# Optimization experiments

Hardware: AMD Instinct MI355X
Metric: run time of the kernel (lower is better)

## Reference

```python
import jax, jax.numpy as jnp
import numpy as np


def setup_inputs() -> dict:
    key = jax.random.key(0)
    k1, k2 = jax.random.split(key)
    B, N, T, D = 16, 2048, 168, 64
    spatial_nodes = jax.random.normal(k1, (B, N, D), dtype=jnp.float32)
    temporal_nodes = jax.random.normal(k2, (B, T, D), dtype=jnp.float32)
    return {"spatial_nodes": spatial_nodes, "temporal_nodes": temporal_nodes}


def reference(spatial_nodes, temporal_nodes):
    # node_embs: [B, N+T, D]
    node_embs = jnp.concatenate([spatial_nodes, temporal_nodes], axis=1)
    # Dense pairwise similarity, then tanh(relu(.)) threshold.
    # batch_adj: [B, N+T, N+T]
    batch_adj = jnp.einsum('bnf,bmf->bnm', node_embs, node_embs)
    batch_adj = jnp.tanh(jax.nn.relu(batch_adj))
    # The torch module additionally extracts per-batch variable-length
    # edge lists (nonzero indices + weights) from batch_adj; those are a
    # pure re-indexing of batch_adj with data-dependent shapes, so the
    # jit-compatible reference returns the dense adjacency, from which
    # edge lists are trivially recoverable (nonzero entries of batch_adj).
    return batch_adj
```

## Files before the change

kernel.cpp:

```cpp
#include <hip/hip_runtime.h>
#include <stdint.h>


constexpr int Bsz = 16;
constexpr int Nsp = 2048;
constexpr int Ttm = 168;
constexpr int D   = 64;
constexpr int M   = Nsp + Ttm;
constexpr int NG32 = (M + 31) / 32;
constexpr int NG   = 72;
constexpr int GRP_SH   = 4 * 64 * 8;
constexpr int BATCH_SH = NG * GRP_SH;
constexpr int PLANE_SH = Bsz * BATCH_SH;
constexpr size_t WS_NEED = (size_t)2 * PLANE_SH * sizeof(unsigned short);

typedef __attribute__((ext_vector_type(8)))  short bf16x8;
typedef __attribute__((ext_vector_type(16))) float f32x16;

__device__ inline void split8(const float4& a, const float4& b,
                              bf16x8& hi, bf16x8& lo) {
    float x[8] = {a.x, a.y, a.z, a.w, b.x, b.y, b.z, b.w};
    #pragma unroll
    for (int i = 0; i < 8; ++i) {
        union { float f; uint32_t u; } v; v.f = x[i];
        uint32_t hu = (v.u + 0x7FFFu + ((v.u >> 16) & 1u)) >> 16;
        union { uint32_t u; float f; } hf; hf.u = hu << 16;
        union { float f; uint32_t u; } r; r.f = x[i] - hf.f;
        uint32_t lu = (r.u + 0x7FFFu + ((r.u >> 16) & 1u)) >> 16;
        hi[i] = (short)hu;
        lo[i] = (short)lu;
    }
}

__device__ inline float act_tanh_relu(float x) {
    const float xr = fmaxf(x, 0.0f);
    const float e  = __expf(2.0f * xr);
    const float r  = __builtin_amdgcn_rcpf(e + 1.0f);
    return 1.0f - 2.0f * r;
}

__global__ __launch_bounds__(256) void convert_kernel(
    const float* __restrict__ spatial,
    const float* __restrict__ temporal,
    unsigned short* __restrict__ ws)
{
    const int idx = blockIdx.x * 256 + threadIdx.x;
    const int b  = idx / (NG * 4 * 64);
    const int r1 = idx % (NG * 4 * 64);
    const int g  = r1 / (4 * 64);
    const int r2 = r1 % (4 * 64);
    const int ks   = r2 >> 6;
    const int lane = r2 & 63;
    const int row  = 32 * g + (lane & 31);
    const int k0   = ks * 16 + 8 * (lane >> 5);

    float4 v0 = make_float4(0.f, 0.f, 0.f, 0.f), v1 = v0;
    if (row < M) {
        const float* src = (row < Nsp)
            ? spatial  + ((size_t)b * Nsp + row) * D
            : temporal + ((size_t)b * Ttm + (row - Nsp)) * D;
        v0 = *(const float4*)(src + k0);
        v1 = *(const float4*)(src + k0 + 4);
    }
    bf16x8 hi, lo;
    split8(v0, v1, hi, lo);

    const size_t o = (size_t)b * BATCH_SH + (size_t)g * GRP_SH + (ks * 64 + lane) * 8;
    *(bf16x8*)(ws + o)            = hi;
    *(bf16x8*)(ws + PLANE_SH + o) = lo;
}

__global__ __launch_bounds__(256, 4) void stgraph_rowpanel(
    const unsigned short* __restrict__ ws,
    float* __restrict__ out)
{
    const int tid = threadIdx.x;
    const int g   = blockIdx.x;
    const int b   = blockIdx.y;

    const int lane = tid & 63;
    const int w    = tid >> 6;
    const int l31  = lane & 31;
    const int lhi  = lane >> 5;

    const unsigned short* Hb = ws + (size_t)b * BATCH_SH;
    const unsigned short* Lb = Hb + PLANE_SH;

    bf16x8 ahi[4], alo[4];
    #pragma unroll
    for (int ks = 0; ks < 4; ++ks) {
        const int fo = (ks * 64 + lane) * 8;
        ahi[ks] = *(const bf16x8*)(Hb + (size_t)g * GRP_SH + fo);
        alo[ks] = *(const bf16x8*)(Lb + (size_t)g * GRP_SH + fo);
    }

    float* out_b = out + (size_t)b * M * M;

    for (int ct = w; ct < NG32; ct += 4) {
        f32x16 acc = {};
        #pragma unroll
        for (int ks = 0; ks < 4; ++ks) {
            const int fo = (ks * 64 + lane) * 8;
            bf16x8 bhi = *(const bf16x8*)(Hb + (size_t)ct * GRP_SH + fo);
            bf16x8 blo = *(const bf16x8*)(Lb + (size_t)ct * GRP_SH + fo);
            acc = __builtin_amdgcn_mfma_f32_32x32x16_bf16(ahi[ks], bhi, acc, 0, 0, 0);
            acc = __builtin_amdgcn_mfma_f32_32x32x16_bf16(ahi[ks], blo, acc, 0, 0, 0);
            acc = __builtin_amdgcn_mfma_f32_32x32x16_bf16(alo[ks], bhi, acc, 0, 0, 0);
        }

        const int col = 32 * ct + l31;
        if (col < M) {
            #pragma unroll
            for (int r = 0; r < 16; ++r) {
                const int grow = 32 * g + (r & 3) + 8 * (r >> 2) + 4 * lhi;
                if (grow < M)
                    out_b[(size_t)grow * M + col] = act_tanh_relu(acc[r]);
            }
        }
    }
}

constexpr int TILE = 128;
constexpr int NT   = (M + TILE - 1) / TILE;
constexpr int NPAIR = NT * (NT + 1) / 2;

__global__ __launch_bounds__(256, 3) void stgraph_fallback(
    const float* __restrict__ spatial,
    const float* __restrict__ temporal,
    float* __restrict__ out)
{
    const int tid = threadIdx.x;
    const int b   = blockIdx.y;
    const int p = blockIdx.x;
    int ti = (int)((37.0f - sqrtf(1369.0f - 8.0f * (float)p)) * 0.5f);
    while (ti * (37 - ti) / 2 > p) --ti;
    while ((ti + 1) * (36 - ti) / 2 <= p) ++ti;
    const int tj = ti + (p - ti * (37 - ti) / 2);
    const bool diag = (ti == tj);

    const float* sp_b = spatial  + (size_t)b * Nsp * D;
    const float* tp_b = temporal + (size_t)b * Ttm * D;

    const int lane = tid & 63;
    const int w    = tid >> 6;
    const int l31  = lane & 31;
    const int lhi  = lane >> 5;

    const int giA = ti * TILE + 32 * w + l31;
    const float* rowA = nullptr;
    if (giA < M)
        rowA = (giA < Nsp) ? sp_b + (size_t)giA * D
                           : tp_b + (size_t)(giA - Nsp) * D;
    const float* rowB[4];
    #pragma unroll
    for (int t = 0; t < 4; ++t) {
        const int gj = tj * TILE + 32 * t + l31;
        rowB[t] = nullptr;
        if (gj < M)
            rowB[t] = (gj < Nsp) ? sp_b + (size_t)gj * D
                                 : tp_b + (size_t)(gj - Nsp) * D;
    }

    f32x16 acc[4] = {};
    #pragma unroll
    for (int ks = 0; ks < 4; ++ks) {
        const int ko = ks * 16 + 8 * lhi;
        float4 a0 = make_float4(0.f, 0.f, 0.f, 0.f), a1 = a0;
        if (rowA) { a0 = *(const float4*)(rowA + ko); a1 = *(const float4*)(rowA + ko + 4); }
        bf16x8 ahi, alo;
        split8(a0, a1, ahi, alo);
        #pragma unroll
        for (int t = 0; t < 4; ++t) {
            float4 b0 = make_float4(0.f, 0.f, 0.f, 0.f), b1 = b0;
            if (rowB[t]) { b0 = *(const float4*)(rowB[t] + ko); b1 = *(const float4*)(rowB[t] + ko + 4); }
            bf16x8 bhi, blo;
            split8(b0, b1, bhi, blo);
            acc[t] = __builtin_amdgcn_mfma_f32_32x32x16_bf16(ahi, bhi, acc[t], 0, 0, 0);
            acc[t] = __builtin_amdgcn_mfma_f32_32x32x16_bf16(ahi, blo, acc[t], 0, 0, 0);
            acc[t] = __builtin_amdgcn_mfma_f32_32x32x16_bf16(alo, bhi, acc[t], 0, 0, 0);
        }
    }

    float* out_b = out + (size_t)b * M * M;
    #pragma unroll
    for (int t = 0; t < 4; ++t) {
        const int gj = tj * TILE + 32 * t + l31;
        float v[16];
        #pragma unroll
        for (int r = 0; r < 16; ++r) v[r] = act_tanh_relu(acc[t][r]);
        if (gj < M) {
            #pragma unroll
            for (int r = 0; r < 16; ++r) {
                const int gi = ti * TILE + 32 * w + (r & 3) + 8 * (r >> 2) + 4 * lhi;
                if (gi < M) out_b[(size_t)gi * M + gj] = v[r];
            }
            if (!diag) {
                #pragma unroll
                for (int gq = 0; gq < 4; ++gq) {
                    const int gibase = ti * TILE + 32 * w + 8 * gq + 4 * lhi;
                    float4 w4 = make_float4(v[4 * gq + 0], v[4 * gq + 1],
                                            v[4 * gq + 2], v[4 * gq + 3]);
                    *(float4*)(&out_b[(size_t)gj * M + gibase]) = w4;
                }
            }
        }
    }
}

extern "C" void kernel_launch(void* const* d_in, const int* in_sizes, int n_in,
                              void* d_out, int out_size, void* d_ws, size_t ws_size,
                              hipStream_t stream) {
    const float* spatial  = (const float*)d_in[0];
    const float* temporal = (const float*)d_in[1];
    float* out = (float*)d_out;

    if (d_ws != nullptr && ws_size >= WS_NEED) {
        unsigned short* ws = (unsigned short*)d_ws;
        {
            dim3 block(256);
            dim3 grid((Bsz * NG * 4 * 64) / 256);
            convert_kernel<<<grid, block, 0, stream>>>(spatial, temporal, ws);
        }
        {
            dim3 block(256);
            dim3 grid(NG32, Bsz);
            stgraph_rowpanel<<<grid, block, 0, stream>>>(ws, out);
        }
    } else {
        dim3 block(256);
        dim3 grid(NPAIR, Bsz);
        stgraph_fallback<<<grid, block, 0, stream>>>(spatial, temporal, out);
    }
}
```

Measured before the change: 409.7 us.

## Share column-tile B fragments across 8 waves via async LDS double buffering

The row-panel GEMM becomes 512-thread blocks. Each of the 8 waves owns its own 32-row group, and each block covers one quarter of the column tiles. The hi and lo B fragments for each column tile are copied from global memory straight into a double-buffered LDS area with global_load_lds, so all 8 waves read them from LDS instead of each wave re-reading them from L2. This cuts redundant global/L2 load traffic. In exchange it adds a block-wide barrier per column tile and changes the grid shape, while the output store pattern, which is likely the dominant cost, stays the same.

```diff
diff --git a/kernel.cpp b/kernel.cpp
--- a/kernel.cpp
+++ b/kernel.cpp
@@ -13,6 +13,8 @@
 constexpr int BATCH_SH = NG * GRP_SH;
 constexpr int PLANE_SH = Bsz * BATCH_SH;
 constexpr size_t WS_NEED = (size_t)2 * PLANE_SH * sizeof(unsigned short);
+constexpr int NPANEL  = 9;
+constexpr int QUARTER = 18;
 
 typedef __attribute__((ext_vector_type(8)))  short bf16x8;
 typedef __attribute__((ext_vector_type(16))) float f32x16;
@@ -70,18 +72,24 @@
     *(bf16x8*)(ws + PLANE_SH + o) = lo;
 }
 
-__global__ __launch_bounds__(256, 4) void stgraph_rowpanel(
+__global__ __launch_bounds__(512, 4) void stgraph_gemm(
     const unsigned short* __restrict__ ws,
     float* __restrict__ out)
 {
-    const int tid = threadIdx.x;
-    const int g   = blockIdx.x;
-    const int b   = blockIdx.y;
+    __shared__ __align__(16) unsigned short lds[2][8 * 512];
+
+    const int tid  = threadIdx.x;
+    const int bx   = blockIdx.x;
+    const int b    = blockIdx.y;
+    const int p    = bx >> 2;
+    const int q    = bx & 3;
+    const int clo  = q * QUARTER;
 
     const int lane = tid & 63;
     const int w    = tid >> 6;
     const int l31  = lane & 31;
     const int lhi  = lane >> 5;
+    const int ga   = p * 8 + w;
 
     const unsigned short* Hb = ws + (size_t)b * BATCH_SH;
     const unsigned short* Lb = Hb + PLANE_SH;
@@ -90,19 +98,36 @@
     #pragma unroll
     for (int ks = 0; ks < 4; ++ks) {
         const int fo = (ks * 64 + lane) * 8;
-        ahi[ks] = *(const bf16x8*)(Hb + (size_t)g * GRP_SH + fo);
-        alo[ks] = *(const bf16x8*)(Lb + (size_t)g * GRP_SH + fo);
+        ahi[ks] = *(const bf16x8*)(Hb + (size_t)ga * GRP_SH + fo);
+        alo[ks] = *(const bf16x8*)(Lb + (size_t)ga * GRP_SH + fo);
     }
 
     float* out_b = out + (size_t)b * M * M;
 
-    for (int ct = w; ct < NG32; ct += 4) {
+    auto stage = [&](int buf, int ct) {
+        const unsigned short* src = ((w >= 4) ? Lb : Hb)
+            + (size_t)ct * GRP_SH + ((w & 3) * 64 + lane) * 8;
+        unsigned short* dst = &lds[buf][w * 512];
+        __builtin_amdgcn_global_load_lds(
+            (const __attribute__((address_space(1))) unsigned int*)src,
+            (__attribute__((address_space(3))) unsigned int*)dst,
+            16, 0, 0);
+    };
+
+    stage(0, clo);
+    __syncthreads();
+
+    int cur = 0;
+    for (int k = 0; k < QUARTER; ++k) {
+        const int ct = clo + k;
+        if (k + 1 < QUARTER) stage(cur ^ 1, ct + 1);
+
+        const unsigned short* L = lds[cur];
         f32x16 acc = {};
         #pragma unroll
         for (int ks = 0; ks < 4; ++ks) {
-            const int fo = (ks * 64 + lane) * 8;
-            bf16x8 bhi = *(const bf16x8*)(Hb + (size_t)ct * GRP_SH + fo);
-            bf16x8 blo = *(const bf16x8*)(Lb + (size_t)ct * GRP_SH + fo);
+            bf16x8 bhi = *(const bf16x8*)(&L[(ks)     * 512 + lane * 8]);
+            bf16x8 blo = *(const bf16x8*)(&L[(4 + ks) * 512 + lane * 8]);
             acc = __builtin_amdgcn_mfma_f32_32x32x16_bf16(ahi[ks], bhi, acc, 0, 0, 0);
             acc = __builtin_amdgcn_mfma_f32_32x32x16_bf16(ahi[ks], blo, acc, 0, 0, 0);
             acc = __builtin_amdgcn_mfma_f32_32x32x16_bf16(alo[ks], bhi, acc, 0, 0, 0);
@@ -111,12 +136,15 @@
         const int col = 32 * ct + l31;
         if (col < M) {
             #pragma unroll
-            for (int r = 0; r < 16; ++r) {
-                const int grow = 32 * g + (r & 3) + 8 * (r >> 2) + 4 * lhi;
+            for (int rr = 0; rr < 16; ++rr) {
+                const int grow = 32 * ga + (rr & 3) + 8 * (rr >> 2) + 4 * lhi;
                 if (grow < M)
-                    out_b[(size_t)grow * M + col] = act_tanh_relu(acc[r]);
+                    out_b[(size_t)grow * M + col] = act_tanh_relu(acc[rr]);
             }
         }
+
+        __syncthreads();
+        cur ^= 1;
     }
 }
 
@@ -222,9 +250,9 @@
             convert_kernel<<<grid, block, 0, stream>>>(spatial, temporal, ws);
         }
         {
-            dim3 block(256);
-            dim3 grid(NG32, Bsz);
-            stgraph_rowpanel<<<grid, block, 0, stream>>>(ws, out);
+            dim3 block(512);
+            dim3 grid(NPANEL * 4, Bsz);
+            stgraph_gemm<<<grid, block, 0, stream>>>(ws, out);
         }
     } else {
         dim3 block(256);
```

Measured after the change: 429.2 us. +4.8%, slower.
